# Performance work log

Hardware: AMD Instinct MI355X
Metric: run time of the kernel (lower is better)

## Reference

```python
import jax, jax.numpy as jnp
import numpy as np

EPS = 1e-7  # tf.keras.backend.epsilon()


def squash(v, axis=-1):
    s = jnp.sum(jnp.square(v), axis=axis, keepdims=True)
    scale = s / (1.0 + s) / jnp.sqrt(s + EPS)
    return scale * v


def setup_inputs() -> dict:
    key = jax.random.key(0)
    k1, k2 = jax.random.split(key)
    B, I, D = 64, 2048, 16   # batch, input_num_capsule, input_dim_capsule
    J, K = 32, 16            # num_capsule, dim_capsule
    inputs = jax.random.normal(k1, (B, I, D), dtype=jnp.float32)
    # glorot_uniform-ish init for W: [in_caps, num_caps, in_dim, dim_caps]
    limit = np.sqrt(6.0 / (D + K)).astype(np.float32)
    W = jax.random.uniform(k2, (I, J, D, K), dtype=jnp.float32, minval=-limit, maxval=limit)
    return {"inputs": inputs, "W": W}


def reference(inputs, W, routings=3):
    # u_hat[b,i,j,:] = inputs[b,i,:] @ W[i,j,:,:]
    u_hat = jnp.einsum('bid,ijdk->bijk', inputs, W)  # [B, I, J, K]
    B, I, J, _ = u_hat.shape
    b = jnp.zeros((B, I, J, 1), dtype=u_hat.dtype)
    outputs = None
    for r in range(routings):
        c = jax.nn.softmax(b, axis=2)                              # [B, I, J, 1]
        outputs = squash(jnp.sum(c * u_hat, axis=1, keepdims=True))  # [B, 1, J, K]
        if r < routings - 1:
            b = b + jnp.sum(u_hat * outputs, axis=-1, keepdims=True)
    return jnp.squeeze(outputs, axis=1)  # [B, J, K]
```

## Files before the change

### kernel.cpp

```cpp
#include <hip/hip_runtime.h>
#include <hip/hip_bf16.h>


#define B_ 64
#define I_ 2048
#define D_ 16
#define J_ 32
#define K_ 16
#define JK 512

typedef __attribute__((ext_vector_type(8))) short short8;
typedef __attribute__((ext_vector_type(4))) float float4v;

__device__ __forceinline__ unsigned short f2bf(float f) {
    union { float f; unsigned int i; } v;
    v.f = f;
    const unsigned int x = v.i;
    return (unsigned short)((x + 0x7fffu + ((x >> 16) & 1u)) >> 16);
}

__device__ __forceinline__ void unpack8(const uint4 r, float* u) {
    union { unsigned int i; float f; } t;
    t.i = r.x << 16;         u[0] = t.f;
    t.i = r.x & 0xffff0000u; u[1] = t.f;
    t.i = r.y << 16;         u[2] = t.f;
    t.i = r.y & 0xffff0000u; u[3] = t.f;
    t.i = r.z << 16;         u[4] = t.f;
    t.i = r.z & 0xffff0000u; u[5] = t.f;
    t.i = r.w << 16;         u[6] = t.f;
    t.i = r.w & 0xffff0000u; u[7] = t.f;
}

__global__ __launch_bounds__(256)
void caps_produce(const float* __restrict__ x, const float* __restrict__ W,
                  unsigned short* __restrict__ uhat) {
    __shared__ unsigned short wlds[32 * 384];
    __shared__ unsigned short zbuf[8];
    __shared__ unsigned short ctile[4][16 * 264];
    const int i = blockIdx.x;
    const int tid = threadIdx.x;

    if (tid < 8) zbuf[tid] = 0;

    {
        const float* wbase = W + (size_t)i * (J_ * D_ * K_);
        const int k = tid & 15;
#pragma unroll
        for (int half = 0; half < 2; ++half) {
            const int j = (tid >> 4) + half * 16;
            const float* p = wbase + j * (D_ * K_) + k;
            float vals[16];
#pragma unroll
            for (int d = 0; d < 16; ++d) vals[d] = p[d * K_];
            unsigned int pk[8];
#pragma unroll
            for (int q = 0; q < 8; ++q)
                pk[q] = ((unsigned int)f2bf(vals[2 * q + 1]) << 16) |
                        f2bf(vals[2 * q]);
            uint4* dst = reinterpret_cast<uint4*>(wlds + j * 384 + k * 24);
            uint4 w0; w0.x = pk[0]; w0.y = pk[1]; w0.z = pk[2]; w0.w = pk[3];
            uint4 w1; w1.x = pk[4]; w1.y = pk[5]; w1.z = pk[6]; w1.w = pk[7];
            dst[0] = w0; dst[1] = w1;
        }
    }
    __syncthreads();

    const int lane = tid & 63;
    const int wv = tid >> 6;
    const int quad = lane >> 4;
    const int l15 = lane & 15;
    const int b = wv * 16 + l15;

    union { uint4 u; short8 s; } bfrag;
    {
        const float* xp = x + ((size_t)b * I_ + i) * D_ + (quad & 1) * 8;
        const float4 x0 = reinterpret_cast<const float4*>(xp)[0];
        const float4 x1 = reinterpret_cast<const float4*>(xp)[1];
        bfrag.u.x = ((unsigned int)f2bf(x0.y) << 16) | f2bf(x0.x);
        bfrag.u.y = ((unsigned int)f2bf(x0.w) << 16) | f2bf(x0.z);
        bfrag.u.z = ((unsigned int)f2bf(x1.y) << 16) | f2bf(x1.x);
        bfrag.u.w = ((unsigned int)f2bf(x1.w) << 16) | f2bf(x1.z);
        if (quad >= 2) { bfrag.u.x = 0; bfrag.u.y = 0; bfrag.u.z = 0; bfrag.u.w = 0; }
    }

    const unsigned short* aptr =
        (quad >= 2) ? zbuf : (wlds + l15 * 24 + (quad & 1) * 8);
    const int astride = (quad >= 2) ? 0 : 384;
    unsigned short* ct = &ctile[wv][0];

    for (int jh = 0; jh < 2; ++jh) {
#pragma unroll
        for (int jj = 0; jj < 16; ++jj) {
            const int j = jh * 16 + jj;
            union { uint4 u; short8 s; } af;
            af.u = *reinterpret_cast<const uint4*>(aptr + (size_t)j * astride);
            float4v acc = {0.f, 0.f, 0.f, 0.f};
            acc = __builtin_amdgcn_mfma_f32_16x16x32_bf16(af.s, bfrag.s, acc,
                                                          0, 0, 0);
            uint2 pk;
            pk.x = ((unsigned int)f2bf(acc[1]) << 16) | f2bf(acc[0]);
            pk.y = ((unsigned int)f2bf(acc[3]) << 16) | f2bf(acc[2]);
            *reinterpret_cast<uint2*>(ct + l15 * 264 + jj * 16 + quad * 4) = pk;
        }
#pragma unroll
        for (int r = 0; r < 8; ++r) {
            const int bsub = r * 2 + (lane >> 5);
            const int c32 = lane & 31;
            const uint4 val = *reinterpret_cast<const uint4*>(
                ct + bsub * 264 + c32 * 8);
            *reinterpret_cast<uint4*>(
                uhat + ((size_t)(wv * 16 + bsub) * I_ + i) * JK + jh * 256 +
                c32 * 8) = val;
        }
    }
}

__global__ __launch_bounds__(256)
void caps_sum0(const unsigned short* __restrict__ uhat,
               float* __restrict__ spart2) {
    __shared__ float part[4][512];
    const int bq = blockIdx.x;
    const int b = bq >> 2, q = bq & 3;
    const int lane = threadIdx.x & 63;
    const int w = threadIdx.x >> 6;

    const unsigned short* up =
        uhat + ((size_t)b * I_ + q * 512 + w * 128) * JK + lane * 8;

    float acc[8];
#pragma unroll
    for (int k = 0; k < 8; ++k) acc[k] = 0.f;

    for (int ii = 0; ii < 128; ii += 4) {
        uint4 r[4];
#pragma unroll
        for (int s = 0; s < 4; ++s)
            r[s] = *reinterpret_cast<const uint4*>(up + (size_t)(ii + s) * JK);
#pragma unroll
        for (int s = 0; s < 4; ++s) {
            float u[8];
            unpack8(r[s], u);
#pragma unroll
            for (int k = 0; k < 8; ++k) acc[k] += u[k];
        }
    }

    float4 o0, o1;
    o0.x = acc[0]; o0.y = acc[1]; o0.z = acc[2]; o0.w = acc[3];
    o1.x = acc[4]; o1.y = acc[5]; o1.z = acc[6]; o1.w = acc[7];
    reinterpret_cast<float4*>(&part[w][lane * 8])[0] = o0;
    reinterpret_cast<float4*>(&part[w][lane * 8])[1] = o1;
    __syncthreads();

    const int t = threadIdx.x;
#pragma unroll
    for (int e = 0; e < 2; ++e) {
        const int jk = t * 2 + e;
        spart2[(size_t)bq * 512 + jk] =
            part[0][jk] + part[1][jk] + part[2][jk] + part[3][jk];
    }
}

__global__ __launch_bounds__(512)
void caps_squash0(const float* __restrict__ spart2, float* __restrict__ vsum) {
    const int bl = blockIdx.x;
    const int jk = threadIdx.x;
    float s = spart2[(size_t)(bl * 4 + 0) * 512 + jk] +
              spart2[(size_t)(bl * 4 + 1) * 512 + jk] +
              spart2[(size_t)(bl * 4 + 2) * 512 + jk] +
              spart2[(size_t)(bl * 4 + 3) * 512 + jk];
    s *= (1.f / 32.f);
    float q = s * s;
    q += __shfl_xor(q, 1, 64);
    q += __shfl_xor(q, 2, 64);
    q += __shfl_xor(q, 4, 64);
    q += __shfl_xor(q, 8, 64);
    const float scale = q / ((1.f + q) * sqrtf(q + 1e-7f));
    vsum[bl * JK + jk] = scale * s;
}

__global__ __launch_bounds__(64)
void caps_route1(const unsigned short* __restrict__ uhat,
                 const float* __restrict__ vsum, float* __restrict__ spart) {
    const int lane = threadIdx.x;
    const int bl = blockIdx.x >> 6;
    const int chunk = blockIdx.x & 63;
    const int h = lane >> 5;
    const int j = lane & 31;

    float v[16];
    {
        const float4* vp =
            reinterpret_cast<const float4*>(vsum + bl * JK + j * 16);
        const float4 a0 = vp[0], a1 = vp[1], a2 = vp[2], a3 = vp[3];
        v[0] = a0.x; v[1] = a0.y; v[2] = a0.z; v[3] = a0.w;
        v[4] = a1.x; v[5] = a1.y; v[6] = a1.z; v[7] = a1.w;
        v[8] = a2.x; v[9] = a2.y; v[10] = a2.z; v[11] = a2.w;
        v[12] = a3.x; v[13] = a3.y; v[14] = a3.z; v[15] = a3.w;
    }

    float acc[16];
#pragma unroll
    for (int k = 0; k < 16; ++k) acc[k] = 0.f;

    const unsigned short* up =
        uhat + ((size_t)bl * I_ + chunk * 32 + h) * JK + j * 16;

    uint4 c0 = reinterpret_cast<const uint4*>(up)[0];
    uint4 c1 = reinterpret_cast<const uint4*>(up)[1];

#pragma unroll 4
    for (int t = 0; t < 16; ++t) {
        uint4 n0, n1;
        if (t < 15) {
            const uint4* np =
                reinterpret_cast<const uint4*>(up + (size_t)(t + 1) * 2 * JK);
            n0 = np[0];
            n1 = np[1];
        }
        float u[16];
        unpack8(c0, u);
        unpack8(c1, u + 8);
        float p = 0.f;
#pragma unroll
        for (int k = 0; k < 16; ++k) p += u[k] * v[k];
        const float e = __expf(p);
        float S = e;
        S += __shfl_xor(S, 1, 64);
        S += __shfl_xor(S, 2, 64);
        S += __shfl_xor(S, 4, 64);
        S += __shfl_xor(S, 8, 64);
        S += __shfl_xor(S, 16, 64);
        const float c = e / S;
#pragma unroll
        for (int k = 0; k < 16; ++k) acc[k] += c * u[k];
        c0 = n0;
        c1 = n1;
    }

#pragma unroll
    for (int k = 0; k < 16; ++k) acc[k] += __shfl_xor(acc[k], 32, 64);

    if (h == 0) {
        float* sp = spart + ((size_t)chunk * B_ + bl) * JK + j * 16;
#pragma unroll
        for (int q = 0; q < 4; ++q) {
            float4 o;
            o.x = acc[q * 4 + 0]; o.y = acc[q * 4 + 1];
            o.z = acc[q * 4 + 2]; o.w = acc[q * 4 + 3];
            reinterpret_cast<float4*>(sp)[q] = o;
        }
    }
}

template <int MODE>
__global__ __launch_bounds__(512)
void caps_squash(const float* __restrict__ spart, float* __restrict__ vsum,
                 float* __restrict__ out) {
    const int bl = blockIdx.x;
    const int jk = threadIdx.x;
    float s = 0.f;
#pragma unroll 8
    for (int p = 0; p < 64; ++p)
        s += spart[((size_t)p * B_ + bl) * JK + jk];
    float q = s * s;
    q += __shfl_xor(q, 1, 64);
    q += __shfl_xor(q, 2, 64);
    q += __shfl_xor(q, 4, 64);
    q += __shfl_xor(q, 8, 64);
    const float scale = q / ((1.f + q) * sqrtf(q + 1e-7f));
    const float v = scale * s;
    if (MODE == 1) vsum[bl * JK + jk] += v;
    else           out[(size_t)bl * JK + jk] = v;
}

extern "C" void kernel_launch(void* const* d_in, const int* in_sizes, int n_in,
                              void* d_out, int out_size, void* d_ws,
                              size_t ws_size, hipStream_t stream) {
    const float* x = (const float*)d_in[0];
    const float* W = (const float*)d_in[1];
    float* out = (float*)d_out;

    char* ws = (char*)d_ws;
    unsigned short* uhat = (unsigned short*)ws;
    float* spart = (float*)(ws + (size_t)B_ * I_ * JK * 2);
    float* vsum = spart + (size_t)64 * B_ * JK;

    caps_produce<<<I_, 256, 0, stream>>>(x, W, uhat);

    caps_sum0<<<256, 256, 0, stream>>>(uhat, spart);
    caps_squash0<<<B_, 512, 0, stream>>>(spart, vsum);

    caps_route1<<<4096, 64, 0, stream>>>(uhat, vsum, spart);
    caps_squash<1><<<B_, 512, 0, stream>>>(spart, vsum, out);

    caps_route1<<<4096, 64, 0, stream>>>(uhat, vsum, spart);
    caps_squash<2><<<B_, 512, 0, stream>>>(spart, vsum, out);
}
```

Before: 202.1 us.

## Reorder produce loads, shrink store tile, widen sum0 grid, use DPP softmax reduction

Several independent changes. In caps_produce the x fragment is now loaded before W is staged, and the output tile is halved to 8 j per group. caps_sum0 runs four times as many blocks, each summing fewer rows, and caps_squash0 now adds 16 partial sums instead of 4. The route kernel's softmax denominator uses a DPP row-shift prefix scan plus readlane in place of xor shuffles. The intent is more parallelism, less LDS per block and cheaper cross-lane reduction, but the DPP scan is only correct if the row-shift and row_bcast sequence and the chosen lanes really produce each half-wave's total.

```diff
diff --git a/kernel.cpp b/kernel.cpp
--- a/kernel.cpp
+++ b/kernel.cpp
@@ -31,39 +31,24 @@
     t.i = r.w & 0xffff0000u; u[7] = t.f;
 }
 
+template <int CTRL>
+__device__ __forceinline__ float dpp_add(float x) {
+    union { float f; int i; } a, b;
+    a.f = x;
+    b.i = __builtin_amdgcn_update_dpp(0, a.i, CTRL, 0xf, 0xf, false);
+    return x + b.f;
+}
+
 __global__ __launch_bounds__(256)
 void caps_produce(const float* __restrict__ x, const float* __restrict__ W,
                   unsigned short* __restrict__ uhat) {
     __shared__ unsigned short wlds[32 * 384];
     __shared__ unsigned short zbuf[8];
-    __shared__ unsigned short ctile[4][16 * 264];
+    __shared__ unsigned short ctile[4][16 * 136];
     const int i = blockIdx.x;
     const int tid = threadIdx.x;
 
     if (tid < 8) zbuf[tid] = 0;
-
-    {
-        const float* wbase = W + (size_t)i * (J_ * D_ * K_);
-        const int k = tid & 15;
-#pragma unroll
-        for (int half = 0; half < 2; ++half) {
-            const int j = (tid >> 4) + half * 16;
-            const float* p = wbase + j * (D_ * K_) + k;
-            float vals[16];
-#pragma unroll
-            for (int d = 0; d < 16; ++d) vals[d] = p[d * K_];
-            unsigned int pk[8];
-#pragma unroll
-            for (int q = 0; q < 8; ++q)
-                pk[q] = ((unsigned int)f2bf(vals[2 * q + 1]) << 16) |
-                        f2bf(vals[2 * q]);
-            uint4* dst = reinterpret_cast<uint4*>(wlds + j * 384 + k * 24);
-            uint4 w0; w0.x = pk[0]; w0.y = pk[1]; w0.z = pk[2]; w0.w = pk[3];
-            uint4 w1; w1.x = pk[4]; w1.y = pk[5]; w1.z = pk[6]; w1.w = pk[7];
-            dst[0] = w0; dst[1] = w1;
-        }
-    }
-    __syncthreads();
 
     const int lane = tid & 63;
     const int wv = tid >> 6;
@@ -83,15 +68,38 @@
         if (quad >= 2) { bfrag.u.x = 0; bfrag.u.y = 0; bfrag.u.z = 0; bfrag.u.w = 0; }
     }
 
+    {
+        const float* wbase = W + (size_t)i * (J_ * D_ * K_);
+        const int k = tid & 15;
+#pragma unroll
+        for (int half = 0; half < 2; ++half) {
+            const int j = (tid >> 4) + half * 16;
+            const float* p = wbase + j * (D_ * K_) + k;
+            float vals[16];
+#pragma unroll
+            for (int d = 0; d < 16; ++d) vals[d] = p[d * K_];
+            unsigned int pk[8];
+#pragma unroll
+            for (int q = 0; q < 8; ++q)
+                pk[q] = ((unsigned int)f2bf(vals[2 * q + 1]) << 16) |
+                        f2bf(vals[2 * q]);
+            uint4* dst = reinterpret_cast<uint4*>(wlds + j * 384 + k * 24);
+            uint4 w0; w0.x = pk[0]; w0.y = pk[1]; w0.z = pk[2]; w0.w = pk[3];
+            uint4 w1; w1.x = pk[4]; w1.y = pk[5]; w1.z = pk[6]; w1.w = pk[7];
+            dst[0] = w0; dst[1] = w1;
+        }
+    }
+    __syncthreads();
+
     const unsigned short* aptr =
         (quad >= 2) ? zbuf : (wlds + l15 * 24 + (quad & 1) * 8);
     const int astride = (quad >= 2) ? 0 : 384;
     unsigned short* ct = &ctile[wv][0];
 
-    for (int jh = 0; jh < 2; ++jh) {
-#pragma unroll
-        for (int jj = 0; jj < 16; ++jj) {
-            const int j = jh * 16 + jj;
+    for (int jg = 0; jg < 4; ++jg) {
+#pragma unroll
+        for (int jj = 0; jj < 8; ++jj) {
+            const int j = jg * 8 + jj;
             union { uint4 u; short8 s; } af;
             af.u = *reinterpret_cast<const uint4*>(aptr + (size_t)j * astride);
             float4v acc = {0.f, 0.f, 0.f, 0.f};
@@ -100,17 +108,17 @@
             uint2 pk;
             pk.x = ((unsigned int)f2bf(acc[1]) << 16) | f2bf(acc[0]);
             pk.y = ((unsigned int)f2bf(acc[3]) << 16) | f2bf(acc[2]);
-            *reinterpret_cast<uint2*>(ct + l15 * 264 + jj * 16 + quad * 4) = pk;
-        }
-#pragma unroll
-        for (int r = 0; r < 8; ++r) {
-            const int bsub = r * 2 + (lane >> 5);
-            const int c32 = lane & 31;
+            *reinterpret_cast<uint2*>(ct + l15 * 136 + jj * 16 + quad * 4) = pk;
+        }
+#pragma unroll
+        for (int r = 0; r < 4; ++r) {
+            const int bsub = r * 4 + (lane >> 4);
+            const int c16 = lane & 15;
             const uint4 val = *reinterpret_cast<const uint4*>(
-                ct + bsub * 264 + c32 * 8);
+                ct + bsub * 136 + c16 * 8);
             *reinterpret_cast<uint4*>(
-                uhat + ((size_t)(wv * 16 + bsub) * I_ + i) * JK + jh * 256 +
-                c32 * 8) = val;
+                uhat + ((size_t)(wv * 16 + bsub) * I_ + i) * JK + jg * 128 +
+                c16 * 8) = val;
         }
     }
 }
@@ -120,18 +128,18 @@
                float* __restrict__ spart2) {
     __shared__ float part[4][512];
     const int bq = blockIdx.x;
-    const int b = bq >> 2, q = bq & 3;
+    const int b = bq >> 4, q = bq & 15;
     const int lane = threadIdx.x & 63;
     const int w = threadIdx.x >> 6;
 
     const unsigned short* up =
-        uhat + ((size_t)b * I_ + q * 512 + w * 128) * JK + lane * 8;
+        uhat + ((size_t)b * I_ + q * 128 + w * 32) * JK + lane * 8;
 
     float acc[8];
 #pragma unroll
     for (int k = 0; k < 8; ++k) acc[k] = 0.f;
 
-    for (int ii = 0; ii < 128; ii += 4) {
+    for (int ii = 0; ii < 32; ii += 4) {
         uint4 r[4];
 #pragma unroll
         for (int s = 0; s < 4; ++s)
@@ -165,10 +173,10 @@
 void caps_squash0(const float* __restrict__ spart2, float* __restrict__ vsum) {
     const int bl = blockIdx.x;
     const int jk = threadIdx.x;
-    float s = spart2[(size_t)(bl * 4 + 0) * 512 + jk] +
-              spart2[(size_t)(bl * 4 + 1) * 512 + jk] +
-              spart2[(size_t)(bl * 4 + 2) * 512 + jk] +
-              spart2[(size_t)(bl * 4 + 3) * 512 + jk];
+    float s = 0.f;
+#pragma unroll
+    for (int p = 0; p < 16; ++p)
+        s += spart2[(size_t)(bl * 16 + p) * 512 + jk];
     s *= (1.f / 32.f);
     float q = s * s;
     q += __shfl_xor(q, 1, 64);
@@ -226,12 +234,17 @@
         for (int k = 0; k < 16; ++k) p += u[k] * v[k];
         const float e = __expf(p);
         float S = e;
-        S += __shfl_xor(S, 1, 64);
-        S += __shfl_xor(S, 2, 64);
-        S += __shfl_xor(S, 4, 64);
-        S += __shfl_xor(S, 8, 64);
-        S += __shfl_xor(S, 16, 64);
-        const float c = e / S;
+        S = dpp_add<0x111>(S);
+        S = dpp_add<0x112>(S);
+        S = dpp_add<0x114>(S);
+        S = dpp_add<0x118>(S);
+        S = dpp_add<0x142>(S);
+        union { float f; int i; } sv, lo, hi;
+        sv.f = S;
+        lo.i = __builtin_amdgcn_readlane(sv.i, 31);
+        hi.i = __builtin_amdgcn_readlane(sv.i, 63);
+        const float Ssel = (h == 0) ? lo.f : hi.f;
+        const float c = e / Ssel;
 #pragma unroll
         for (int k = 0; k < 16; ++k) acc[k] += c * u[k];
         c0 = n0;
@@ -288,7 +301,7 @@
 
     caps_produce<<<I_, 256, 0, stream>>>(x, W, uhat);
 
-    caps_sum0<<<256, 256, 0, stream>>>(uhat, spart);
+    caps_sum0<<<1024, 256, 0, stream>>>(uhat, spart);
     caps_squash0<<<B_, 512, 0, stream>>>(spart, vsum);
 
     caps_route1<<<4096, 64, 0, stream>>>(uhat, vsum, spart);
```

New measurement: 195.2 us. 3.4% less time.
